# Kernel optimization log

Measured on AMD Instinct MI355X. Metric: run time of the kernel, lower is better.

## Reference

```python
import jax, jax.numpy as jnp
import numpy as np

INPUT_DIM = 64
LATENT_DIM = 512
K = 32
BATCH = 262144


def xavier_uniform(key, shape):
    fan_out, fan_in = shape
    limit = float(np.sqrt(6.0 / (fan_in + fan_out)))
    return jax.random.uniform(key, shape, jnp.float32, -limit, limit)


def setup_inputs() -> dict:
    key = jax.random.key(0)
    kx, ke, kd = jax.random.split(key, 3)
    x = jax.random.normal(kx, (BATCH, INPUT_DIM), dtype=jnp.float32)
    enc_W = xavier_uniform(ke, (LATENT_DIM, INPUT_DIM))  # torch Linear weight layout [out, in]
    enc_b = jnp.zeros((LATENT_DIM,), jnp.float32)
    dec_W = xavier_uniform(kd, (INPUT_DIM, LATENT_DIM))
    dec_b = jnp.zeros((INPUT_DIM,), jnp.float32)
    return {"x": x, "enc_W": enc_W, "enc_b": enc_b, "dec_W": dec_W, "dec_b": dec_b}


def reference(x, enc_W, enc_b, dec_W, dec_b):
    # encode: linear -> relu -> top-k mask
    z = jax.nn.relu(x @ enc_W.T + enc_b)                 # [B, LATENT_DIM]
    vals, idx = jax.lax.top_k(z, K)                      # [B, K]
    rows = jnp.arange(z.shape[0])[:, None]               # [B, 1]
    z_sparse = jnp.zeros_like(z).at[rows, idx].set(vals) # scatter top-k back
    # decode
    x_hat = z_sparse @ dec_W.T + dec_b                   # [B, INPUT_DIM]
    return x_hat, z_sparse
```

## Files before the change

### kernel.cpp

```cpp
#include <hip/hip_runtime.h>


#define BATCH 262144
#define IND   64
#define LAT   512
#define TOPK  32
#define RPB   128
#define TR    32
#define NTT   (RPB / TR)
#define CCAP  64
#define EPSC  3.5e-5f
#define NB    32
#define NBPAD 36

typedef __attribute__((ext_vector_type(8))) short short8;
typedef __attribute__((ext_vector_type(4))) float f32x4;

__device__ __forceinline__ unsigned short f2bf(float f) {
  unsigned u = __float_as_uint(f);
  unsigned r = ((u >> 16) & 1u) + 0x7FFFu;
  return (unsigned short)((u + r) >> 16);
}
__device__ __forceinline__ float bfbits2f(unsigned short s) {
  return __uint_as_float(((unsigned)s) << 16);
}
__device__ __forceinline__ float edgef(int t) {
  return __uint_as_float((unsigned)(1888 + t) << 19);
}
__device__ __forceinline__ short8 pack8(float4 a, float4 b) {
  short8 r;
  r[0] = (short)f2bf(a.x); r[1] = (short)f2bf(a.y);
  r[2] = (short)f2bf(a.z); r[3] = (short)f2bf(a.w);
  r[4] = (short)f2bf(b.x); r[5] = (short)f2bf(b.y);
  r[6] = (short)f2bf(b.z); r[7] = (short)f2bf(b.w);
  return r;
}
__device__ __forceinline__ void split8(const float* p, short8& h, short8& l) {
  #pragma unroll
  for (int i = 0; i < 8; i++) {
    float v = p[i];
    unsigned short hb = f2bf(v);
    float r = v - bfbits2f(hb);
    h[i] = (short)hb;
    l[i] = (short)f2bf(r);
  }
}

__global__ __launch_bounds__(256, 2)
void sae_fused(const float* __restrict__ xg,
               const float* __restrict__ encW,
               const float* __restrict__ encB,
               const float* __restrict__ decW,
               const float* __restrict__ decB,
               float* __restrict__ out_xhat,
               float* __restrict__ out_z)
{
  __shared__ union {
    struct {
      unsigned hist[TR][NBPAD];
      unsigned fb[256];
    } h;
    unsigned short zsp[TR][520];
  } u;
  __shared__ float    xtile[TR][68];
  __shared__ float    cval[TR][CCAP];
  __shared__ int      cidx[TR][CCAP];
  __shared__ float    rowlo[TR];
  __shared__ float    rowep[TR];
  __shared__ float    xabs[TR];
  __shared__ float    xlo0[TR];
  __shared__ float    xinvw[TR];
  __shared__ float    xwid[TR];
  __shared__ int      ccnt[TR];
  __shared__ int      degen[TR];
  __shared__ int      wmax_i;
  __shared__ int      fbmask;

  const int tid  = threadIdx.x;
  const int w    = tid >> 6;
  const int lane = tid & 63;
  const int c    = lane & 15;
  const int q    = lane >> 4;

  if (tid == 0) wmax_i = 0;
  __syncthreads();

  short8 beh[8][2], bel[8][2];
  float  lmax = 0.0f;
  #pragma unroll
  for (int n = 0; n < 8; n++)
    #pragma unroll
    for (int ks = 0; ks < 2; ks++) {
      const float* p = encW + (size_t)(128*w + 16*n + c)*IND + 32*ks + 8*q;
      #pragma unroll
      for (int i = 0; i < 8; i++) lmax = fmaxf(lmax, fabsf(p[i]));
      split8(p, beh[n][ks], bel[n][ks]);
    }
  atomicMax(&wmax_i, __float_as_int(lmax));

  float ebias[8];
  #pragma unroll
  for (int n = 0; n < 8; n++) ebias[n] = encB[128*w + 16*n + c];
  const float dbias = decB[16*w + c];
  __syncthreads();
  const float wmaxf = __int_as_float(wmax_i);

  #pragma unroll 1
  for (int t = 0; t < NTT; t++) {
    const int rowbase = blockIdx.x * RPB + t * TR;

    {
      uint4 z4 = {0,0,0,0};
      uint4* hp = (uint4*)&u.h.hist[0][0];
      hp[tid] = z4;
      if (tid < 96) hp[256 + tid] = z4;
      if (tid < TR) { ccnt[tid] = 0; degen[tid] = 0; }
      if (tid == 0) fbmask = 0;
    }
    {
      const int row = tid >> 3, sub = tid & 7;
      const f32x4* gp = (const f32x4*)(xg + (size_t)(rowbase + row)*IND) + 2*sub;
      f32x4 a = __builtin_nontemporal_load(gp);
      f32x4 b = __builtin_nontemporal_load(gp + 1);
      *(f32x4*)&xtile[row][8*sub]     = a;
      *(f32x4*)&xtile[row][8*sub + 4] = b;
      float s  = fabsf(a.x)+fabsf(a.y)+fabsf(a.z)+fabsf(a.w)
               + fabsf(b.x)+fabsf(b.y)+fabsf(b.z)+fabsf(b.w);
      float s2 = a.x*a.x+a.y*a.y+a.z*a.z+a.w*a.w
               + b.x*b.x+b.y*b.y+b.z*b.z+b.w*b.w;
      s  += __shfl_xor(s, 1);  s  += __shfl_xor(s, 2);  s  += __shfl_xor(s, 4);
      s2 += __shfl_xor(s2, 1); s2 += __shfl_xor(s2, 2); s2 += __shfl_xor(s2, 4);
      if (sub == 0) {
        xabs[row] = s;
        const float sig = 0.058926f * sqrtf(s2);
        xlo0[row]  = fmaxf(0.7f * sig, edgef(1));
        xwid[row]  = (2.5f / (float)NB) * sig;
        xinvw[row] = (float)NB / fmaxf(2.5f * sig, 1e-20f);
      }
    }
    __syncthreads();

    f32x4 acc[2][8];
    #pragma unroll
    for (int m2 = 0; m2 < 2; m2++)
      #pragma unroll
      for (int n = 0; n < 8; n++) acc[m2][n] = (f32x4){0.f,0.f,0.f,0.f};

    #pragma unroll
    for (int m2 = 0; m2 < 2; m2++) {
      const float* xr = &xtile[16*m2 + c][0];
      short8 a0h, a0l, a1h, a1l;
      split8(xr + 8*q,      a0h, a0l);
      split8(xr + 32 + 8*q, a1h, a1l);
      #pragma unroll
      for (int n = 0; n < 8; n++) {
        acc[m2][n] = __builtin_amdgcn_mfma_f32_16x16x32_bf16(a0h, beh[n][0], acc[m2][n], 0,0,0);
        acc[m2][n] = __builtin_amdgcn_mfma_f32_16x16x32_bf16(a0l, beh[n][0], acc[m2][n], 0,0,0);
        acc[m2][n] = __builtin_amdgcn_mfma_f32_16x16x32_bf16(a0h, bel[n][0], acc[m2][n], 0,0,0);
        acc[m2][n] = __builtin_amdgcn_mfma_f32_16x16x32_bf16(a1h, beh[n][1], acc[m2][n], 0,0,0);
        acc[m2][n] = __builtin_amdgcn_mfma_f32_16x16x32_bf16(a1l, beh[n][1], acc[m2][n], 0,0,0);
        acc[m2][n] = __builtin_amdgcn_mfma_f32_16x16x32_bf16(a1h, bel[n][1], acc[m2][n], 0,0,0);
      }
    }
    {
      float flo[2][4], fiw[2][4];
      #pragma unroll
      for (int m2 = 0; m2 < 2; m2++)
        #pragma unroll
        for (int r = 0; r < 4; r++) {
          flo[m2][r] = xlo0[16*m2 + 4*q + r];
          fiw[m2][r] = xinvw[16*m2 + 4*q + r];
        }
      #pragma unroll
      for (int m2 = 0; m2 < 2; m2++)
        #pragma unroll
        for (int n = 0; n < 8; n++)
          #pragma unroll
          for (int r = 0; r < 4; r++) {
            float v = fmaxf(acc[m2][n][r] + ebias[n], 0.0f);
            acc[m2][n][r] = v;
            if (v >= flo[m2][r]) {
              const int row = 16*m2 + 4*q + r;
              int k = (int)((v - flo[m2][r]) * fiw[m2][r]);
              k = min(k, NB-1);
              atomicAdd(&u.h.hist[row][k], 1u);
            }
          }
    }
    __syncthreads();

    #pragma unroll 1
    for (int rr = 0; rr < 8; rr++) {
      const int row = 8*w + rr;
      uint4 h = {0,0,0,0};
      if (lane < 8) h = *(const uint4*)&u.h.hist[row][4*lane];
      int T = (int)(h.x + h.y + h.z + h.w);
      int I = T;
      #pragma unroll
      for (int d = 1; d < 8; d <<= 1) {
        int t2 = __shfl_down(I, d);
        if (lane + d < 8) I += t2;
      }
      const int I0 = __shfl(I, 0);
      if (I0 < TOPK) {
        if (lane == 0) atomicOr(&fbmask, (int)(1u << row));
      } else {
        unsigned long long msk = __ballot(I >= TOPK);
        const int ls = __popcll(msk) - 1;
        const int Il = __shfl(I, ls);
        const int hx = __shfl((int)h.x, ls);
        const int hy = __shfl((int)h.y, ls);
        const int hz = __shfl((int)h.z, ls);
        const int s1 = Il - hx, s2 = s1 - hy, s3 = s2 - hz;
        const int t8 = (s3 >= TOPK) ? 4*ls+3 : (s2 >= TOPK) ? 4*ls+2
                     : (s1 >= TOPK) ? 4*ls+1 : 4*ls;
        if (lane == 0) {
          const float eps2 = EPSC * wmaxf * xabs[row] + 1e-7f;
          rowep[row] = eps2;
          rowlo[row] = fmaxf(xlo0[row] + (float)t8 * xwid[row] - 2.0f*eps2, 1e-30f);
        }
      }
    }
    __syncthreads();

    if (fbmask) {
      unsigned fbm = (unsigned)fbmask;
      while (fbm) {
        const int R = (int)__ffs(fbm) - 1;
        fbm &= fbm - 1;
        u.h.fb[tid] = 0;
        __syncthreads();
        if ((lane >> 4) == ((R >> 2) & 3)) {
          const int m2R = R >> 4, rR = R & 3;
          #pragma unroll
          for (int m2 = 0; m2 < 2; m2++)
            #pragma unroll
            for (int r = 0; r < 4; r++)
              if (m2 == m2R && r == rR) {
                #pragma unroll
                for (int n = 0; n < 8; n++) {
                  float v = acc[m2][n][r];
                  int k8 = (int)(__float_as_uint(v) >> 19) - 1888;
                  k8 = max(0, min(255, k8));
                  atomicAdd(&u.h.fb[k8], 1u);
                }
              }
        }
        __syncthreads();
        if (w == 0) {
          uint4 h = *(const uint4*)&u.h.fb[4*lane];
          int T = (int)(h.x + h.y + h.z + h.w);
          int I = T;
          #pragma unroll
          for (int d = 1; d < 64; d <<= 1) {
            int t2 = __shfl_down(I, d);
            if (lane + d < 64) I += t2;
          }
          const int I0  = __shfl(I, 0);
          const int hx0 = __shfl((int)h.x, 0);
          if (I0 - hx0 < TOPK) {
            if (lane == 0) { degen[R] = 1; rowlo[R] = edgef(1); rowep[R] = 0.f; }
          } else {
            unsigned long long msk = __ballot(I >= TOPK);
            const int ls = __popcll(msk) - 1;
            const int Il = __shfl(I, ls);
            const int hx = __shfl((int)h.x, ls);
            const int hy = __shfl((int)h.y, ls);
            const int hz = __shfl((int)h.z, ls);
            const int s1 = Il - hx, s2 = s1 - hy, s3 = s2 - hz;
            const int t8 = (s3 >= TOPK) ? 4*ls+3 : (s2 >= TOPK) ? 4*ls+2
                         : (s1 >= TOPK) ? 4*ls+1 : 4*ls;
            if (lane == 0) {
              const float eps2 = EPSC * wmaxf * xabs[R] + 1e-7f;
              rowep[R] = eps2;
              rowlo[R] = fmaxf(edgef(t8) - 2.0f*eps2, 1e-30f);
            }
          }
        }
        __syncthreads();
      }
    }

    {
      uint4 z4 = {0,0,0,0};
      uint4* zp = (uint4*)&u.zsp[0][0];
      #pragma unroll
      for (int i = 0; i < 8; i++) zp[tid + 256*i] = z4;
      if (tid < 32) zp[2048 + tid] = z4;
    }
    __syncthreads();

    #pragma unroll
    for (int m2 = 0; m2 < 2; m2++)
      #pragma unroll
      for (int r = 0; r < 4; r++) {
        const int row = 16*m2 + 4*q + r;
        const float lo = rowlo[row];
        const int dg = degen[row];
        #pragma unroll
        for (int n = 0; n < 8; n++) {
          const float v = acc[m2][n][r];
          if (v >= lo) {
            if (dg) {
              u.zsp[row][128*w + 16*n + c] = f2bf(v);
            } else {
              int slot = atomicAdd(&ccnt[row], 1);
              if (slot < CCAP) { cval[row][slot] = v; cidx[row][slot] = 128*w + 16*n + c; }
            }
          }
        }
      }
    __syncthreads();

    #pragma unroll 1
    for (int rr = 0; rr < 8; rr++) {
      const int row = 8*w + rr;
      if (!degen[row]) {
        const int m = min(ccnt[row], CCAP);
        float cv = (lane < m) ? cval[row][lane] : -1e30f;
        int   ci = (lane < m) ? cidx[row][lane] : 0x7FFFFFFF;
        int rank = 0;
        for (int jj = 0; jj < m; jj++) {
          const float vj = __shfl(cv, jj);
          const int   ij = __shfl(ci, jj);
          rank += (vj > cv || (vj == cv && ij < ci)) ? 1 : 0;
        }
        bool kept = (lane < m) && (rank < TOPK);
        float kv = kept ? cv : 1e30f;
        float uv = (!kept && lane < m) ? cv : -1e30f;
        #pragma unroll
        for (int d = 1; d < 64; d <<= 1) {
          kv = fminf(kv, __shfl_xor(kv, d));
          uv = fmaxf(uv, __shfl_xor(uv, d));
        }
        if (kv - uv < 2.0f*rowep[row]) {
          const int js = (lane < m) ? ci : 0;
          const float* wr = encW + (size_t)js * IND;
          const float* xr = &xtile[row][0];
          float s = 0.0f;
          #pragma unroll 1
          for (int g4 = 0; g4 < 4; g4++) {
            const float4 w0 = *(const float4*)(wr + 16*g4);
            const float4 w1 = *(const float4*)(wr + 16*g4 + 4);
            const float4 w2 = *(const float4*)(wr + 16*g4 + 8);
            const float4 w3 = *(const float4*)(wr + 16*g4 + 12);
            const float* xk = xr + 16*g4;
            s = fmaf(xk[0],  w0.x, s); s = fmaf(xk[1],  w0.y, s);
            s = fmaf(xk[2],  w0.z, s); s = fmaf(xk[3],  w0.w, s);
            s = fmaf(xk[4],  w1.x, s); s = fmaf(xk[5],  w1.y, s);
            s = fmaf(xk[6],  w1.z, s); s = fmaf(xk[7],  w1.w, s);
            s = fmaf(xk[8],  w2.x, s); s = fmaf(xk[9],  w2.y, s);
            s = fmaf(xk[10], w2.z, s); s = fmaf(xk[11], w2.w, s);
            s = fmaf(xk[12], w3.x, s); s = fmaf(xk[13], w3.y, s);
            s = fmaf(xk[14], w3.z, s); s = fmaf(xk[15], w3.w, s);
          }
          s += encB[js];
          s = fmaxf(s, 0.0f);
          const float val = (lane < m) ? s : -1e30f;
          rank = 0;
          for (int jj = 0; jj < m; jj++) {
            const float vj = __shfl(val, jj);
            const int   ij = __shfl(ci, jj);
            rank += (vj > val || (vj == val && ij < ci)) ? 1 : 0;
          }
          kept = (lane < m) && (rank < TOPK);
          cv = val;
        }
        if (kept) u.zsp[row][ci] = f2bf(cv);
      }
    }
    __syncthreads();

    #pragma unroll 1
    for (int rr = 0; rr < 8; rr++) {
      const int row = 8*w + rr;
      const unsigned short* zr = &u.zsp[row][8*lane];
      f32x4 o0, o1;
      o0.x = bfbits2f(zr[0]); o0.y = bfbits2f(zr[1]); o0.z = bfbits2f(zr[2]); o0.w = bfbits2f(zr[3]);
      o1.x = bfbits2f(zr[4]); o1.y = bfbits2f(zr[5]); o1.z = bfbits2f(zr[6]); o1.w = bfbits2f(zr[7]);
      f32x4* orow = (f32x4*)(out_z + (size_t)(rowbase + row)*LAT + 8*lane);
      __builtin_nontemporal_store(o0, orow);
      __builtin_nontemporal_store(o1, orow + 1);
    }
    {
      f32x4 acc2[2];
      acc2[0] = (f32x4){0.f,0.f,0.f,0.f};
      acc2[1] = (f32x4){0.f,0.f,0.f,0.f};
      const float* pw = decW + (size_t)(16*w + c)*LAT + 8*q;
      #pragma unroll 1
      for (int g = 0; g < 4; g++) {
        short8 bd4[4];
        #pragma unroll
        for (int j = 0; j < 4; j++) {
          const float* p = pw + 32*(4*g + j);
          bd4[j] = pack8(*(const float4*)p, *(const float4*)(p + 4));
        }
        #pragma unroll
        for (int j = 0; j < 4; j++) {
          const int ks = 4*g + j;
          short8 a0 = *(const short8*)&u.zsp[c][32*ks + 8*q];
          short8 a1 = *(const short8*)&u.zsp[16 + c][32*ks + 8*q];
          acc2[0] = __builtin_amdgcn_mfma_f32_16x16x32_bf16(a0, bd4[j], acc2[0], 0,0,0);
          acc2[1] = __builtin_amdgcn_mfma_f32_16x16x32_bf16(a1, bd4[j], acc2[1], 0,0,0);
        }
      }
      #pragma unroll
      for (int m2 = 0; m2 < 2; m2++)
        #pragma unroll
        for (int r = 0; r < 4; r++)
          out_xhat[(size_t)(rowbase + 16*m2 + 4*q + r)*IND + 16*w + c] = acc2[m2][r] + dbias;
    }
    __syncthreads();
  }
}

extern "C" void kernel_launch(void* const* d_in, const int* in_sizes, int n_in,
                              void* d_out, int out_size, void* d_ws, size_t ws_size,
                              hipStream_t stream) {
  (void)in_sizes; (void)n_in; (void)out_size; (void)d_ws; (void)ws_size;
  const float* x    = (const float*)d_in[0];
  const float* encW = (const float*)d_in[1];
  const float* encB = (const float*)d_in[2];
  const float* decW = (const float*)d_in[3];
  const float* decB = (const float*)d_in[4];
  float* out_xhat = (float*)d_out;
  float* out_z    = out_xhat + (size_t)BATCH * IND;

  dim3 grid(BATCH / RPB), block(256);
  sae_fused<<<grid, block, 0, stream>>>(x, encW, encB, decW, decB, out_xhat, out_z);
}
```

Baseline: 1.715 ms.

## Split LDS union to zero sparse tile early, fully unroll decoder loads

```diff
diff --git a/kernel.cpp b/kernel.cpp
--- a/kernel.cpp
+++ b/kernel.cpp
@@ -46,7 +46,8 @@
   }
 }
 
-__global__ __launch_bounds__(256, 2)
+__global__ __launch_bounds__(256)
+__attribute__((amdgpu_waves_per_eu(2, 2)))
 void sae_fused(const float* __restrict__ xg,
                const float* __restrict__ encW,
                const float* __restrict__ encB,
@@ -55,16 +56,12 @@
                float* __restrict__ out_xhat,
                float* __restrict__ out_z)
 {
-  __shared__ union {
-    struct {
-      unsigned hist[TR][NBPAD];
-      unsigned fb[256];
-    } h;
-    unsigned short zsp[TR][520];
-  } u;
+  __shared__ unsigned       hist[TR][NBPAD];
+  __shared__ unsigned       fb[256];
+  __shared__ unsigned short zsp[TR][520];
   __shared__ float    xtile[TR][68];
   __shared__ float    cval[TR][CCAP];
-  __shared__ int      cidx[TR][CCAP];
+  __shared__ unsigned short cidx[TR][CCAP];
   __shared__ float    rowlo[TR];
   __shared__ float    rowep[TR];
   __shared__ float    xabs[TR];
@@ -111,9 +108,13 @@
 
     {
       uint4 z4 = {0,0,0,0};
-      uint4* hp = (uint4*)&u.h.hist[0][0];
+      uint4* hp = (uint4*)&hist[0][0];
       hp[tid] = z4;
-      if (tid < 96) hp[256 + tid] = z4;
+      if (tid < 32) hp[256 + tid] = z4;
+      uint4* zp = (uint4*)&zsp[0][0];
+      #pragma unroll
+      for (int i = 0; i < 8; i++) zp[tid + 256*i] = z4;
+      if (tid < 32) zp[2048 + tid] = z4;
       if (tid < TR) { ccnt[tid] = 0; degen[tid] = 0; }
       if (tid == 0) fbmask = 0;
     }
@@ -183,7 +184,7 @@
               const int row = 16*m2 + 4*q + r;
               int k = (int)((v - flo[m2][r]) * fiw[m2][r]);
               k = min(k, NB-1);
-              atomicAdd(&u.h.hist[row][k], 1u);
+              atomicAdd(&hist[row][k], 1u);
             }
           }
     }
@@ -193,7 +194,7 @@
     for (int rr = 0; rr < 8; rr++) {
       const int row = 8*w + rr;
       uint4 h = {0,0,0,0};
-      if (lane < 8) h = *(const uint4*)&u.h.hist[row][4*lane];
+      if (lane < 8) h = *(const uint4*)&hist[row][4*lane];
       int T = (int)(h.x + h.y + h.z + h.w);
       int I = T;
       #pragma unroll
@@ -228,7 +229,7 @@
       while (fbm) {
         const int R = (int)__ffs(fbm) - 1;
         fbm &= fbm - 1;
-        u.h.fb[tid] = 0;
+        fb[tid] = 0;
         __syncthreads();
         if ((lane >> 4) == ((R >> 2) & 3)) {
           const int m2R = R >> 4, rR = R & 3;
@@ -242,13 +243,13 @@
                   float v = acc[m2][n][r];
                   int k8 = (int)(__float_as_uint(v) >> 19) - 1888;
                   k8 = max(0, min(255, k8));
-                  atomicAdd(&u.h.fb[k8], 1u);
+                  atomicAdd(&fb[k8], 1u);
                 }
               }
         }
         __syncthreads();
         if (w == 0) {
-          uint4 h = *(const uint4*)&u.h.fb[4*lane];
+          uint4 h = *(const uint4*)&fb[4*lane];
           int T = (int)(h.x + h.y + h.z + h.w);
           int I = T;
           #pragma unroll
@@ -281,15 +282,6 @@
       }
     }
 
-    {
-      uint4 z4 = {0,0,0,0};
-      uint4* zp = (uint4*)&u.zsp[0][0];
-      #pragma unroll
-      for (int i = 0; i < 8; i++) zp[tid + 256*i] = z4;
-      if (tid < 32) zp[2048 + tid] = z4;
-    }
-    __syncthreads();
-
     #pragma unroll
     for (int m2 = 0; m2 < 2; m2++)
       #pragma unroll
@@ -302,10 +294,13 @@
           const float v = acc[m2][n][r];
           if (v >= lo) {
             if (dg) {
-              u.zsp[row][128*w + 16*n + c] = f2bf(v);
+              zsp[row][128*w + 16*n + c] = f2bf(v);
             } else {
               int slot = atomicAdd(&ccnt[row], 1);
-              if (slot < CCAP) { cval[row][slot] = v; cidx[row][slot] = 128*w + 16*n + c; }
+              if (slot < CCAP) {
+                cval[row][slot] = v;
+                cidx[row][slot] = (unsigned short)(128*w + 16*n + c);
+              }
             }
           }
         }
@@ -318,7 +313,7 @@
       if (!degen[row]) {
         const int m = min(ccnt[row], CCAP);
         float cv = (lane < m) ? cval[row][lane] : -1e30f;
-        int   ci = (lane < m) ? cidx[row][lane] : 0x7FFFFFFF;
+        int   ci = (lane < m) ? (int)cidx[row][lane] : 0x7FFFFFFF;
         int rank = 0;
         for (int jj = 0; jj < m; jj++) {
           const float vj = __shfl(cv, jj);
@@ -366,7 +361,7 @@
           kept = (lane < m) && (rank < TOPK);
           cv = val;
         }
-        if (kept) u.zsp[row][ci] = f2bf(cv);
+        if (kept) zsp[row][ci] = f2bf(cv);
       }
     }
     __syncthreads();
@@ -374,7 +369,7 @@
     #pragma unroll 1
     for (int rr = 0; rr < 8; rr++) {
       const int row = 8*w + rr;
-      const unsigned short* zr = &u.zsp[row][8*lane];
+      const unsigned short* zr = &zsp[row][8*lane];
       f32x4 o0, o1;
       o0.x = bfbits2f(zr[0]); o0.y = bfbits2f(zr[1]); o0.z = bfbits2f(zr[2]); o0.w = bfbits2f(zr[3]);
       o1.x = bfbits2f(zr[4]); o1.y = bfbits2f(zr[5]); o1.z = bfbits2f(zr[6]); o1.w = bfbits2f(zr[7]);
@@ -383,26 +378,21 @@
       __builtin_nontemporal_store(o1, orow + 1);
     }
     {
+      short8 bd[16];
+      #pragma unroll
+      for (int ks = 0; ks < 16; ks++) {
+        const float* p = decW + (size_t)(16*w + c)*LAT + 32*ks + 8*q;
+        bd[ks] = pack8(*(const float4*)p, *(const float4*)(p + 4));
+      }
       f32x4 acc2[2];
       acc2[0] = (f32x4){0.f,0.f,0.f,0.f};
       acc2[1] = (f32x4){0.f,0.f,0.f,0.f};
-      const float* pw = decW + (size_t)(16*w + c)*LAT + 8*q;
-      #pragma unroll 1
-      for (int g = 0; g < 4; g++) {
-        short8 bd4[4];
-        #pragma unroll
-        for (int j = 0; j < 4; j++) {
-          const float* p = pw + 32*(4*g + j);
-          bd4[j] = pack8(*(const float4*)p, *(const float4*)(p + 4));
-        }
-        #pragma unroll
-        for (int j = 0; j < 4; j++) {
-          const int ks = 4*g + j;
-          short8 a0 = *(const short8*)&u.zsp[c][32*ks + 8*q];
-          short8 a1 = *(const short8*)&u.zsp[16 + c][32*ks + 8*q];
-          acc2[0] = __builtin_amdgcn_mfma_f32_16x16x32_bf16(a0, bd4[j], acc2[0], 0,0,0);
-          acc2[1] = __builtin_amdgcn_mfma_f32_16x16x32_bf16(a1, bd4[j], acc2[1], 0,0,0);
-        }
+      #pragma unroll
+      for (int ks = 0; ks < 16; ks++) {
+        short8 a0 = *(const short8*)&zsp[c][32*ks + 8*q];
+        short8 a1 = *(const short8*)&zsp[16 + c][32*ks + 8*q];
+        acc2[0] = __builtin_amdgcn_mfma_f32_16x16x32_bf16(a0, bd[ks], acc2[0], 0,0,0);
+        acc2[1] = __builtin_amdgcn_mfma_f32_16x16x32_bf16(a1, bd[ks], acc2[1], 0,0,0);
       }
       #pragma unroll
       for (int m2 = 0; m2 < 2; m2++)
```

New measurement: 1.786 ms. +4.1%, slower.
